# Optimization experiments

Measured on AMD Instinct MI355X. Metric: run time of the kernel, lower is better.

## Reference

```python
import jax, jax.numpy as jnp
import numpy as np

B, C, T, H, W = 32, 384, 16, 14, 14
K, NUM_SAMPLES, SIGMA = 8, 1000, 0.05
C2 = 2 * C  # ScoreNet doubles embed_dim internally


def setup_inputs() -> dict:
    key = jax.random.key(0)
    ks = jax.random.split(key, 12)
    def rn(k, shape, s=0.02):
        return jax.random.normal(k, shape, dtype=jnp.float32) * s
    return {
        "frames": jax.random.normal(ks[0], (B, C, T, H, W), dtype=jnp.float32),
        "noise": jax.random.normal(ks[1], (B, NUM_SAMPLES, T), dtype=jnp.float32),
        "conv_w": rn(ks[2], (C, C, 1, 3, 3)),
        "conv_b": jnp.zeros((C,), jnp.float32),
        "bn_g": jnp.ones((C,), jnp.float32),
        "bn_b": jnp.zeros((C,), jnp.float32),
        "ln_g": jnp.ones((C2,), jnp.float32),
        "ln_b": jnp.zeros((C2,), jnp.float32),
        "lin_w": rn(ks[3], (C2, C2)),
        "lin_b": jnp.zeros((C2,), jnp.float32),
        "w1": rn(ks[4], (C2, C)), "b1": jnp.zeros((C,), jnp.float32),
        "w2": rn(ks[5], (C, C // 2)), "b2": jnp.zeros((C // 2,), jnp.float32),
        "w3": rn(ks[6], (C // 2, 1)), "b3": jnp.zeros((1,), jnp.float32),
    }


def score_net(frames, conv_w, conv_b, bn_g, bn_b, ln_g, ln_b, lin_w, lin_b,
              w1, b1, w2, b2, w3, b3):
    x = jax.lax.stop_gradient(frames)  # ScoreNet detaches its input
    x = jax.lax.conv_general_dilated(
        x, conv_w, window_strides=(1, 2, 2), padding='VALID',
        dimension_numbers=('NCDHW', 'OIDHW', 'NCDHW'))
    x = x + conv_b[None, :, None, None, None]
    # BatchNorm3d in training mode: biased batch stats over (N,T,H,W)
    m = x.mean(axis=(0, 2, 3, 4))
    v = x.var(axis=(0, 2, 3, 4))
    x = (x - m[None, :, None, None, None]) / jnp.sqrt(v + 1e-5)[None, :, None, None, None]
    x = x * bn_g[None, :, None, None, None] + bn_b[None, :, None, None, None]
    # b c t h w -> b t (h w) c
    b, c, t, h, w = x.shape
    x = jnp.transpose(x, (0, 2, 3, 4, 1)).reshape(b, t, h * w, c)
    x = jnp.concatenate([x.mean(axis=2), x.max(axis=2)], axis=-1)  # [B,T,2C]
    # LayerNorm(2C)
    mu = x.mean(-1, keepdims=True)
    var = x.var(-1, keepdims=True)
    x = (x - mu) / jnp.sqrt(var + 1e-5) * ln_g + ln_b
    x = jax.nn.gelu(x @ lin_w + lin_b, approximate=False)
    local_x = x[..., :C2 // 2]
    global_x = jnp.broadcast_to(x[..., C2 // 2:].mean(axis=1, keepdims=True), (b, t, C2 // 2))
    x = jnp.concatenate([local_x, global_x], axis=-1)
    x = jax.nn.gelu(x @ w1 + b1, approximate=False)
    x = jax.nn.gelu(x @ w2 + b2, approximate=False)
    score = (x @ w3 + b3)[..., 0]  # [B,T]
    smin = score.min(axis=-1, keepdims=True)
    smax = score.max(axis=-1, keepdims=True)
    return (score - smin) / (smax - smin + 1e-5)


def perturbed_indicators(score, noise):
    d = score.shape[-1]
    pert = score[:, None, :] + noise * SIGMA  # [B,N,T]
    idx_top = jnp.sort(jax.lax.top_k(pert, K)[1], axis=-1)        # [B,N,K]
    idx_back = jnp.sort(jax.lax.top_k(-pert, d - K)[1], axis=-1)  # [B,N,T-K]
    ind_top = jax.nn.one_hot(idx_top, d, dtype=jnp.float32).mean(axis=1)   # [B,K,T]
    ind_back = jax.nn.one_hot(idx_back, d, dtype=jnp.float32).mean(axis=1)  # [B,T-K,T]
    return ind_top, ind_back


def reference(frames, noise, conv_w, conv_b, bn_g, bn_b, ln_g, ln_b, lin_w, lin_b,
              w1, b1, w2, b2, w3, b3):
    score = score_net(frames, conv_w, conv_b, bn_g, bn_b, ln_g, ln_b, lin_w, lin_b,
                      w1, b1, w2, b2, w3, b3)  # [B,T]
    ind_top, ind_back = perturbed_indicators(score, noise)
    # b c t h w -> b t (h w c)
    flat = jnp.transpose(frames, (0, 2, 3, 4, 1)).reshape(B, T, H * W * C)
    p_top = jnp.einsum('bkd,bdc->bkc', ind_top, flat)
    p_back = jnp.einsum('bkd,bdc->bkc', ind_back, flat)
    frames_topk = jnp.transpose(p_top.reshape(B, K, H, W, C), (0, 4, 1, 2, 3))
    frames_back = jnp.transpose(p_back.reshape(B, T - K, H, W, C), (0, 4, 1, 2, 3))
    sorted_inds = jnp.argsort(score, axis=1)
    return frames_topk, frames_back, sorted_inds
```

## Files before the change

### kernel.cpp

```cpp
#include <hip/hip_runtime.h>
#include <hip/hip_bf16.h>
#include <cstdint>

#define NB 32
#define NC 384
#define NT 16
#define NH 14
#define NW 14
#define HWI 196
#define HOW 6
#define HWO 36
#define C2 768
#define MCONV (NB*NT*HWO)
#define KCONV 3456
#define TOPK 8
#define NSAMP 1000
#define OUT_TOPK_ELEMS (NB*NC*TOPK*HWI)
#define OUT_INDS_OFF   (2*OUT_TOPK_ELEMS)
#define PELEMS (MCONV*NC)

#define OFF_FHI  0ull
#define OFF_FLO  77070336ull
#define OFF_WHI  154140672ull
#define OFF_WLO  156794880ull
#define OFF_CONV 159449088ull
#define OFF_PART 0ull
#define OFF_BNSC 442368ull
#define OFF_BNSH 443904ull
#define OFF_Y    445440ull
#define OFF_X1   2018304ull
#define OFF_GM   3591168ull
#define OFF_H1   3640320ull
#define OFF_H2   4426752ull
#define OFF_IND  4819968ull

typedef __attribute__((ext_vector_type(4))) float f32x4;
typedef __attribute__((ext_vector_type(8))) short bf16x8;

__device__ __forceinline__ unsigned short f2bf(float f) {
  unsigned u = __float_as_uint(f);
  unsigned r = (u + 0x7FFFu + ((u >> 16) & 1u)) >> 16;
  return (unsigned short)r;
}
__device__ __forceinline__ float bf2f(unsigned short u) {
  return __uint_as_float(((unsigned)u) << 16);
}

__device__ __forceinline__ void gload_lds16(const void* gptr, void* lptr) {
  __builtin_amdgcn_global_load_lds(
      (const __attribute__((address_space(1))) unsigned int*)gptr,
      (__attribute__((address_space(3))) unsigned int*)lptr, 16, 0, 0);
}

__global__ __launch_bounds__(256)
void split_all(const float* __restrict__ fr, const float* __restrict__ cw,
               unsigned short* __restrict__ fhi, unsigned short* __restrict__ flo,
               unsigned short* __restrict__ whi, unsigned short* __restrict__ wlo) {
  __shared__ char smem[64 * 197 * 4];
  int bid = blockIdx.x;
  if (bid < 3072) {
    unsigned int (*tile)[197] = (unsigned int (*)[197])smem;
    int cb = bid % 6, bt = bid / 6;
    int b = bt >> 4, t = bt & 15;
    const float* src = fr + (((size_t)b * NC + cb * 64) * NT + t) * HWI;
    for (int i = threadIdx.x; i < 64 * 49; i += 256) {
      int c = i / 49, q = i - c * 49;
      float4 v = *(const float4*)(src + (size_t)c * (NT * HWI) + q * 4);
      float vv[4] = {v.x, v.y, v.z, v.w};
#pragma unroll
      for (int u = 0; u < 4; ++u) {
        unsigned short h = f2bf(vv[u]);
        unsigned short l = f2bf(vv[u] - bf2f(h));
        tile[c][q * 4 + u] = ((unsigned)h << 16) | (unsigned)l;
      }
    }
    __syncthreads();
    size_t obase = ((size_t)bt * HWI) * NC + cb * 64;
    for (int i = threadIdx.x; i < 196 * 8; i += 256) {
      int hw = i >> 3, c8 = i & 7;
      bf16x8 vh, vl;
#pragma unroll
      for (int u = 0; u < 8; ++u) {
        unsigned p = tile[c8 * 8 + u][hw];
        vh[u] = (short)(p >> 16);
        vl[u] = (short)(p & 0xffff);
      }
      size_t o = obase + (size_t)hw * NC + c8 * 8;
      *(bf16x8*)(fhi + o) = vh;
      *(bf16x8*)(flo + o) = vl;
    }
  } else {
    float* t = (float*)smem;
    int co = bid - 3072;
    const float* src = cw + (size_t)co * KCONV;
    for (int i = threadIdx.x; i < KCONV / 4; i += 256)
      *(float4*)&t[i * 4] = *(const float4*)&src[i * 4];
    __syncthreads();
    unsigned short* oh = whi + (size_t)co * KCONV;
    unsigned short* ol = wlo + (size_t)co * KCONV;
    for (int i = threadIdx.x; i < KCONV; i += 256) {
      int c9 = i / NC, ci = i - c9 * NC;
      float v = t[ci * 9 + c9];
      unsigned short h = f2bf(v);
      oh[i] = h; ol[i] = f2bf(v - bf2f(h));
    }
  }
}

__global__ __launch_bounds__(256, 4)
void conv_gemm(const unsigned short* __restrict__ fhi,
               const unsigned short* __restrict__ flo,
               const unsigned short* __restrict__ whi,
               const unsigned short* __restrict__ wlo,
               const float* __restrict__ conv_b,
               float* __restrict__ p0, float* __restrict__ p1,
               float* __restrict__ p2, float* __restrict__ p3) {
  __shared__ unsigned short sAhi[128 * 32], sAlo[128 * 32];
  __shared__ unsigned short sBhi[128 * 32], sBlo[128 * 32];
  const int tid = threadIdx.x;
  const int lane = tid & 63;
  const int wv = tid >> 6;
  const int bid = blockIdx.x;
  const int bm = bid % 144;
  const int r  = bid / 144;
  const int bn = r % 3;
  const int kz = r / 3;

  int aoff[2], boff[2];
#pragma unroll
  for (int j = 0; j < 2; ++j) {
    int l = (wv * 2 + j) * 64 + lane;
    int row = l >> 2;
    int chunk = (l & 3) ^ ((l >> 3) & 3);
    int m = bm * 128 + row;
    int wo = m % 6; int tmp = m / 6;
    int ho = tmp % 6; tmp /= 6;
    aoff[j] = ((tmp * HWI) + (2 * ho) * NW + 2 * wo) * NC + chunk * 8;
    int co = bn * 128 + row;
    boff[j] = co * KCONV + chunk * 8;
  }

  f32x4 acc[4][4];
#pragma unroll
  for (int i = 0; i < 4; ++i)
#pragma unroll
    for (int j = 0; j < 4; ++j) acc[i][j] = (f32x4){0.f, 0.f, 0.f, 0.f};

  const int wrow = (wv >> 1) * 64;
  const int wcol = (wv & 1) * 64;
  const int fr_row = lane & 15;
  const int slot8 = (((lane >> 4) ^ ((fr_row >> 1) & 3))) * 8;

  int c9  = (kz * 27) / 12;
  int rem = (kz * 27) % 12;
  for (int s = 0; s < 27; ++s) {
    int kh = c9 / 3, kw = c9 - kh * 3;
    int soffA = (kh * NW + kw) * NC + rem * 32;
    int soffB = c9 * NC + rem * 32;
#pragma unroll
    for (int j = 0; j < 2; ++j) {
      char* ldsA  = (char*)sAhi + (wv * 2 + j) * 1024;
      char* ldsAl = (char*)sAlo + (wv * 2 + j) * 1024;
      char* ldsB  = (char*)sBhi + (wv * 2 + j) * 1024;
      char* ldsBl = (char*)sBlo + (wv * 2 + j) * 1024;
      gload_lds16(fhi + aoff[j] + soffA, ldsA);
      gload_lds16(flo + aoff[j] + soffA, ldsAl);
      gload_lds16(whi + boff[j] + soffB, ldsB);
      gload_lds16(wlo + boff[j] + soffB, ldsBl);
    }
    __syncthreads();
    bf16x8 ah[4], al[4], bh[4], bl[4];
#pragma unroll
    for (int m = 0; m < 4; ++m) {
      int rr = wrow + m * 16 + fr_row;
      ah[m] = *(const bf16x8*)&sAhi[rr * 32 + slot8];
      al[m] = *(const bf16x8*)&sAlo[rr * 32 + slot8];
    }
#pragma unroll
    for (int n = 0; n < 4; ++n) {
      int rr = wcol + n * 16 + fr_row;
      bh[n] = *(const bf16x8*)&sBhi[rr * 32 + slot8];
      bl[n] = *(const bf16x8*)&sBlo[rr * 32 + slot8];
    }
#pragma unroll
    for (int m = 0; m < 4; ++m)
#pragma unroll
      for (int n = 0; n < 4; ++n) {
        acc[m][n] = __builtin_amdgcn_mfma_f32_16x16x32_bf16(ah[m], bh[n], acc[m][n], 0, 0, 0);
        acc[m][n] = __builtin_amdgcn_mfma_f32_16x16x32_bf16(ah[m], bl[n], acc[m][n], 0, 0, 0);
        acc[m][n] = __builtin_amdgcn_mfma_f32_16x16x32_bf16(al[m], bh[n], acc[m][n], 0, 0, 0);
      }
    __syncthreads();
    if (++rem == 12) { rem = 0; ++c9; }
  }

  float* dst = (kz == 0) ? p0 : (kz == 1) ? p1 : (kz == 2) ? p2 : p3;
#pragma unroll
  for (int m = 0; m < 4; ++m)
#pragma unroll
    for (int n = 0; n < 4; ++n) {
      int col = bn * 128 + wcol + n * 16 + (lane & 15);
      float cb = (kz == 0) ? conv_b[col] : 0.f;
#pragma unroll
      for (int j = 0; j < 4; ++j) {
        int row = bm * 128 + wrow + m * 16 + (lane >> 4) * 4 + j;
        dst[(size_t)row * NC + col] = acc[m][n][j] + cb;
      }
    }
}

__global__ __launch_bounds__(384)
void bn_part(float* __restrict__ p0, const float* __restrict__ p1,
             const float* __restrict__ p2, const float* __restrict__ p3,
             float* __restrict__ part) {
  int c = threadIdx.x;
  int r0 = blockIdx.x * 128;
  float s = 0.f, sq = 0.f;
  for (int r = 0; r < 128; ++r) {
    size_t off = (size_t)(r0 + r) * NC + c;
    float v = p0[off] + p1[off] + p2[off] + p3[off];
    p0[off] = v;
    s += v; sq += v * v;
  }
  part[blockIdx.x * 768 + c] = s;
  part[blockIdx.x * 768 + 384 + c] = sq;
}

__global__ __launch_bounds__(384)
void bn_fin(const float* __restrict__ part, const float* __restrict__ bn_g,
            const float* __restrict__ bn_b, float* __restrict__ bnsc,
            float* __restrict__ bnsh) {
  int c = threadIdx.x;
  float s = 0.f, sq = 0.f;
  for (int i = 0; i < 144; ++i) {
    s += part[i * 768 + c];
    sq += part[i * 768 + 384 + c];
  }
  float mean = s / (float)MCONV;
  float var = sq / (float)MCONV - mean * mean;
  float sc = bn_g[c] / sqrtf(var + 1e-5f);
  bnsc[c] = sc;
  bnsh[c] = bn_b[c] - mean * sc;
}

__global__ __launch_bounds__(384)
void pool_ln(const float* __restrict__ csum,
             const float* __restrict__ bnsc,
             const float* __restrict__ bnsh, const float* __restrict__ ln_g,
             const float* __restrict__ ln_b, float* __restrict__ y) {
  __shared__ float r1[6], r2[6], stats[2];
  int bt = blockIdx.x, c = threadIdx.x;
  float sc = bnsc[c], sh = bnsh[c];
  size_t base = (size_t)bt * HWO * NC + c;
  float sum = 0.f, mx = -1e30f;
#pragma unroll
  for (int hw = 0; hw < HWO; ++hw) {
    float v = csum[base + (size_t)hw * NC] * sc + sh;
    sum += v;
    mx = fmaxf(mx, v);
  }
  float meanv = sum * (1.f / 36.f);
  float v1 = meanv + mx;
  float v2 = meanv * meanv + mx * mx;
#pragma unroll
  for (int off = 32; off; off >>= 1) {
    v1 += __shfl_down(v1, off, 64);
    v2 += __shfl_down(v2, off, 64);
  }
  if ((c & 63) == 0) { r1[c >> 6] = v1; r2[c >> 6] = v2; }
  __syncthreads();
  if (c == 0) {
    float S1 = 0.f, S2 = 0.f;
#pragma unroll
    for (int i = 0; i < 6; ++i) { S1 += r1[i]; S2 += r2[i]; }
    float mu = S1 / (float)C2;
    float var = S2 / (float)C2 - mu * mu;
    stats[0] = mu;
    stats[1] = 1.0f / sqrtf(var + 1e-5f);
  }
  __syncthreads();
  float mu = stats[0], rstd = stats[1];
  y[(size_t)bt * C2 + c] = (meanv - mu) * rstd * ln_g[c] + ln_b[c];
  y[(size_t)bt * C2 + 384 + c] = (mx - mu) * rstd * ln_g[384 + c] + ln_b[384 + c];
}

template <int GELU, int X2, int GM>
__global__ __launch_bounds__(256)
void gemm64(const float* __restrict__ A, const float* __restrict__ gmv,
            const float* __restrict__ Wm,
            const float* __restrict__ bias, float* __restrict__ Cm,
            int K, int N, float* __restrict__ gmout) {
  __shared__ float As[64][17];
  __shared__ float Bs[16][68];
  __shared__ float gmred[16][64];
  int tid = threadIdx.x;
  int tx = tid & 15, ty = tid >> 4;
  int m0 = blockIdx.y * 64, n0 = blockIdx.x * 64;
  int ar = tid >> 2, ak = (tid & 3) * 4;
  int br = tid >> 4, bc = (tid & 15) * 4;
  float acc[4][4] = {};
  for (int kt = 0; kt < K; kt += 16) {
    int kcol = kt + ak;
    float4 av;
    if (X2 && kcol >= 384)
      av = *(const float4*)(gmv + ((m0 + ar) >> 4) * 384 + (kcol - 384));
    else
      av = *(const float4*)(A + (size_t)(m0 + ar) * K + kcol);
    float4 bv = *(const float4*)(Wm + (size_t)(kt + br) * N + n0 + bc);
    As[ar][ak + 0] = av.x; As[ar][ak + 1] = av.y;
    As[ar][ak + 2] = av.z; As[ar][ak + 3] = av.w;
    Bs[br][bc + 0] = bv.x; Bs[br][bc + 1] = bv.y;
    Bs[br][bc + 2] = bv.z; Bs[br][bc + 3] = bv.w;
    __syncthreads();
#pragma unroll
    for (int kk = 0; kk < 16; ++kk) {
      float a0 = As[ty * 4 + 0][kk], a1 = As[ty * 4 + 1][kk];
      float a2 = As[ty * 4 + 2][kk], a3 = As[ty * 4 + 3][kk];
      float b0 = Bs[kk][tx * 4 + 0], b1 = Bs[kk][tx * 4 + 1];
      float b2 = Bs[kk][tx * 4 + 2], b3 = Bs[kk][tx * 4 + 3];
      acc[0][0] += a0 * b0; acc[0][1] += a0 * b1; acc[0][2] += a0 * b2; acc[0][3] += a0 * b3;
      acc[1][0] += a1 * b0; acc[1][1] += a1 * b1; acc[1][2] += a1 * b2; acc[1][3] += a1 * b3;
      acc[2][0] += a2 * b0; acc[2][1] += a2 * b1; acc[2][2] += a2 * b2; acc[2][3] += a2 * b3;
      acc[3][0] += a3 * b0; acc[3][1] += a3 * b1; acc[3][2] += a3 * b2; acc[3][3] += a3 * b3;
    }
    __syncthreads();
  }
  float vout[4][4];
#pragma unroll
  for (int i = 0; i < 4; ++i) {
    int row = m0 + ty * 4 + i;
#pragma unroll
    for (int j = 0; j < 4; ++j) {
      int col = n0 + tx * 4 + j;
      float v = acc[i][j] + bias[col];
      if (GELU) v = 0.5f * v * (1.0f + erff(v * 0.70710678118654752f));
      vout[i][j] = v;
      Cm[(size_t)row * N + col] = v;
    }
  }
  if (GM && n0 >= 384) {
#pragma unroll
    for (int j = 0; j < 4; ++j)
      gmred[ty][tx * 4 + j] = vout[0][j] + vout[1][j] + vout[2][j] + vout[3][j];
    __syncthreads();
    int b_l = tid >> 6, col = tid & 63;
    float g = (gmred[b_l * 4 + 0][col] + gmred[b_l * 4 + 1][col] +
               gmred[b_l * 4 + 2][col] + gmred[b_l * 4 + 3][col]) * (1.f / 16.f);
    gmout[(blockIdx.y * 4 + b_l) * 384 + (n0 - 384) + col] = g;
  }
}

__global__ __launch_bounds__(256)
void score_head(const float* __restrict__ h2, const float* __restrict__ w3,
                const float* __restrict__ b3, const float* __restrict__ noise,
                float* __restrict__ ind, float* __restrict__ out_inds) {
  int b = blockIdx.x;
  int tid = threadIdx.x;
  int lane = tid & 63, wv = tid >> 6;
  __shared__ float sv[16], sn[16];
  __shared__ unsigned cnt[256];
  for (int t = wv; t < 16; t += 4) {
    const float* hr = h2 + ((size_t)b * 16 + t) * 192;
    float p = 0.f;
    for (int i = lane; i < 192; i += 64) p += hr[i] * w3[i];
#pragma unroll
    for (int off = 32; off; off >>= 1) p += __shfl_down(p, off, 64);
    if (lane == 0) sv[t] = p + b3[0];
  }
  cnt[tid] = 0;
  __syncthreads();
  if (tid == 0) {
    float mn = sv[0], mx = sv[0];
    for (int t = 1; t < 16; ++t) { mn = fminf(mn, sv[t]); mx = fmaxf(mx, sv[t]); }
    float inv = 1.0f / (mx - mn + 1e-5f);
    for (int t = 0; t < 16; ++t) sn[t] = (sv[t] - mn) * inv;
  }
  __syncthreads();
  if (tid < 16) {
    int t = tid, r = 0;
    for (int u = 0; u < 16; ++u)
      r += (sv[u] < sv[t]) || (sv[u] == sv[t] && u < t);
    out_inds[b * 16 + r] = (float)t;
  }
  for (int s = tid; s < NSAMP; s += 256) {
    const float* nz = noise + ((size_t)b * NSAMP + s) * 16;
    float pert[16];
#pragma unroll
    for (int t = 0; t < 16; ++t) pert[t] = sn[t] + 0.05f * nz[t];
    unsigned tm = 0, bm2 = 0;
#pragma unroll
    for (int t = 0; t < 16; ++t) {
      int ct = 0, cb = 0;
#pragma unroll
      for (int u = 0; u < 16; ++u) {
        ct += (pert[u] > pert[t]) || (pert[u] == pert[t] && u < t);
        cb += (pert[u] < pert[t]) || (pert[u] == pert[t] && u < t);
      }
      if (ct < 8) tm |= 1u << t;
      if (cb < 8) bm2 |= 1u << t;
    }
    int j = 0, jb = 0;
#pragma unroll
    for (int t = 0; t < 16; ++t) {
      if (tm & (1u << t)) { if (j < 8) atomicAdd(&cnt[j * 16 + t], 1u); ++j; }
      if (bm2 & (1u << t)) { if (jb < 8) atomicAdd(&cnt[128 + jb * 16 + t], 1u); ++jb; }
    }
  }
  __syncthreads();
  ind[b * 256 + tid] = (float)cnt[tid] / 1000.0f;
}

__global__ __launch_bounds__(256)
void gather_k(const float* __restrict__ frames, const float* __restrict__ ind,
              float* __restrict__ out) {
  int bid = blockIdx.x;
  int tid = threadIdx.x;
  int b = (bid * 4) / NC;
  __shared__ float wt[256];
  wt[tid] = ind[b * 256 + tid];
  __syncthreads();
  if (tid >= 196) return;
  int cc = tid / 49, q = tid - cc * 49;
  int bc = bid * 4 + cc;
  const float4* src = (const float4*)(frames + (size_t)bc * NT * HWI) + q;
  float4 v[16];
#pragma unroll
  for (int t = 0; t < 16; ++t) v[t] = src[t * 49];
  float4* o1 = (float4*)(out + (size_t)bc * TOPK * HWI) + q;
  float4* o2 = (float4*)(out + OUT_TOPK_ELEMS + (size_t)bc * TOPK * HWI) + q;
#pragma unroll
  for (int k = 0; k < TOPK; ++k) {
    float4 st = {0.f, 0.f, 0.f, 0.f}, sb = {0.f, 0.f, 0.f, 0.f};
#pragma unroll
    for (int t = 0; t < 16; ++t) {
      float a = wt[k * 16 + t], bw = wt[128 + k * 16 + t];
      st.x += a * v[t].x; st.y += a * v[t].y; st.z += a * v[t].z; st.w += a * v[t].w;
      sb.x += bw * v[t].x; sb.y += bw * v[t].y; sb.z += bw * v[t].z; sb.w += bw * v[t].w;
    }
    o1[k * 49] = st;
    o2[k * 49] = sb;
  }
}

extern "C" void kernel_launch(void* const* d_in, const int* in_sizes, int n_in,
                              void* d_out, int out_size, void* d_ws, size_t ws_size,
                              hipStream_t stream) {
  const float* frames = (const float*)d_in[0];
  const float* noise  = (const float*)d_in[1];
  const float* conv_w = (const float*)d_in[2];
  const float* conv_b = (const float*)d_in[3];
  const float* bn_g   = (const float*)d_in[4];
  const float* bn_b   = (const float*)d_in[5];
  const float* ln_g   = (const float*)d_in[6];
  const float* ln_b   = (const float*)d_in[7];
  const float* lin_w  = (const float*)d_in[8];
  const float* lin_b  = (const float*)d_in[9];
  const float* w1     = (const float*)d_in[10];
  const float* b1     = (const float*)d_in[11];
  const float* w2     = (const float*)d_in[12];
  const float* b2     = (const float*)d_in[13];
  const float* w3     = (const float*)d_in[14];
  const float* b3     = (const float*)d_in[15];

  char* ws = (char*)d_ws;
  unsigned short* fhi = (unsigned short*)(ws + OFF_FHI);
  unsigned short* flo = (unsigned short*)(ws + OFF_FLO);
  unsigned short* whi = (unsigned short*)(ws + OFF_WHI);
  unsigned short* wlo = (unsigned short*)(ws + OFF_WLO);
  float* p0    = (float*)(ws + OFF_CONV);
  float* part  = (float*)(ws + OFF_PART);
  float* bnsc  = (float*)(ws + OFF_BNSC);
  float* bnsh  = (float*)(ws + OFF_BNSH);
  float* y     = (float*)(ws + OFF_Y);
  float* x1    = (float*)(ws + OFF_X1);
  float* gm    = (float*)(ws + OFF_GM);
  float* h1    = (float*)(ws + OFF_H1);
  float* h2    = (float*)(ws + OFF_H2);
  float* ind   = (float*)(ws + OFF_IND);
  float* out   = (float*)d_out;
  float* p1    = out;
  float* p2    = out + PELEMS;
  float* p3    = out + 2 * (size_t)PELEMS;

  split_all<<<3456, 256, 0, stream>>>(frames, conv_w, fhi, flo, whi, wlo);
  conv_gemm<<<1728, 256, 0, stream>>>(fhi, flo, whi, wlo, conv_b, p0, p1, p2, p3);
  bn_part<<<144, 384, 0, stream>>>(p0, p1, p2, p3, part);
  bn_fin<<<1, 384, 0, stream>>>(part, bn_g, bn_b, bnsc, bnsh);
  pool_ln<<<512, 384, 0, stream>>>(p0, bnsc, bnsh, ln_g, ln_b, y);
  gemm64<1, 0, 1><<<dim3(12, 8), 256, 0, stream>>>(y, nullptr, lin_w, lin_b, x1, 768, 768, gm);
  gemm64<1, 1, 0><<<dim3(6, 8), 256, 0, stream>>>(x1, gm, w1, b1, h1, 768, 384, nullptr);
  gemm64<1, 0, 0><<<dim3(3, 8), 256, 0, stream>>>(h1, nullptr, w2, b2, h2, 384, 192, nullptr);
  score_head<<<32, 256, 0, stream>>>(h2, w3, b3, noise, ind, out + OUT_INDS_OFF);
  gather_k<<<3072, 256, 0, stream>>>(frames, ind, out);
}
```

Before: 508.8 us.

## Fuse split-K reduction with pooling stats, remap conv blocks, split score sampling

The split-K partial sums are now reduced in a per-(b,t) kernel that also emits per-channel sum, sum of squares, max and min. This removes the write-back of the reduced conv output and the second full read in pool_ln, which now applies the BN affine to the pooled stats and picks max or min depending on the scale's sign. The conv GEMM block index is remapped so neighbouring blocks land differently across the hardware, and score_head is split across 8 blocks per batch with partial counts summed in gather_k. The sign trick relies on BN being monotone per channel, and bn_fin now reads 512 partial rows instead of 144.

```diff
diff --git a/kernel.cpp b/kernel.cpp
--- a/kernel.cpp
+++ b/kernel.cpp
@@ -24,15 +24,18 @@
 #define OFF_WHI  154140672ull
 #define OFF_WLO  156794880ull
 #define OFF_CONV 159449088ull
-#define OFF_PART 0ull
-#define OFF_BNSC 442368ull
-#define OFF_BNSH 443904ull
-#define OFF_Y    445440ull
-#define OFF_X1   2018304ull
-#define OFF_GM   3591168ull
-#define OFF_H1   3640320ull
-#define OFF_H2   4426752ull
-#define OFF_IND  4819968ull
+#define OFF_SARR 0ull
+#define OFF_SQAR 786432ull
+#define OFF_MXAR 1572864ull
+#define OFF_MNAR 2359296ull
+#define OFF_BNSC 3145728ull
+#define OFF_BNSH 3147264ull
+#define OFF_Y    3148800ull
+#define OFF_X1   4721664ull
+#define OFF_GM   6294528ull
+#define OFF_H1   6343680ull
+#define OFF_H2   7130112ull
+#define OFF_PCNT 7523328ull
 
 typedef __attribute__((ext_vector_type(4))) float f32x4;
 typedef __attribute__((ext_vector_type(8))) short bf16x8;
@@ -121,8 +124,10 @@
   const int lane = tid & 63;
   const int wv = tid >> 6;
   const int bid = blockIdx.x;
-  const int bm = bid % 144;
-  const int r  = bid / 144;
+  const int x  = bid & 7;
+  const int i_ = bid >> 3;
+  const int bm = x * 18 + (i_ % 18);
+  const int r  = i_ / 18;
   const int bn = r % 3;
   const int kz = r / 3;
 
@@ -210,31 +215,34 @@
 }
 
 __global__ __launch_bounds__(384)
-void bn_part(float* __restrict__ p0, const float* __restrict__ p1,
-             const float* __restrict__ p2, const float* __restrict__ p3,
-             float* __restrict__ part) {
-  int c = threadIdx.x;
-  int r0 = blockIdx.x * 128;
-  float s = 0.f, sq = 0.f;
-  for (int r = 0; r < 128; ++r) {
-    size_t off = (size_t)(r0 + r) * NC + c;
+void reduce_all(const float* __restrict__ p0, const float* __restrict__ p1,
+                const float* __restrict__ p2, const float* __restrict__ p3,
+                float* __restrict__ sarr, float* __restrict__ sqarr,
+                float* __restrict__ mxarr, float* __restrict__ mnarr) {
+  int bt = blockIdx.x, c = threadIdx.x;
+  size_t base = (size_t)bt * HWO * NC + c;
+  float s = 0.f, sq = 0.f, mx = -3.4e38f, mn = 3.4e38f;
+#pragma unroll 6
+  for (int hw = 0; hw < HWO; ++hw) {
+    size_t off = base + (size_t)hw * NC;
     float v = p0[off] + p1[off] + p2[off] + p3[off];
-    p0[off] = v;
     s += v; sq += v * v;
-  }
-  part[blockIdx.x * 768 + c] = s;
-  part[blockIdx.x * 768 + 384 + c] = sq;
+    mx = fmaxf(mx, v); mn = fminf(mn, v);
+  }
+  int o = bt * NC + c;
+  sarr[o] = s; sqarr[o] = sq; mxarr[o] = mx; mnarr[o] = mn;
 }
 
 __global__ __launch_bounds__(384)
-void bn_fin(const float* __restrict__ part, const float* __restrict__ bn_g,
-            const float* __restrict__ bn_b, float* __restrict__ bnsc,
-            float* __restrict__ bnsh) {
+void bn_fin(const float* __restrict__ sarr, const float* __restrict__ sqarr,
+            const float* __restrict__ bn_g, const float* __restrict__ bn_b,
+            float* __restrict__ bnsc, float* __restrict__ bnsh) {
   int c = threadIdx.x;
   float s = 0.f, sq = 0.f;
-  for (int i = 0; i < 144; ++i) {
-    s += part[i * 768 + c];
-    sq += part[i * 768 + 384 + c];
+#pragma unroll 8
+  for (int i = 0; i < 512; ++i) {
+    s += sarr[i * NC + c];
+    sq += sqarr[i * NC + c];
   }
   float mean = s / (float)MCONV;
   float var = sq / (float)MCONV - mean * mean;
@@ -244,24 +252,19 @@
 }
 
 __global__ __launch_bounds__(384)
-void pool_ln(const float* __restrict__ csum,
-             const float* __restrict__ bnsc,
-             const float* __restrict__ bnsh, const float* __restrict__ ln_g,
-             const float* __restrict__ ln_b, float* __restrict__ y) {
+void pool_ln(const float* __restrict__ sarr, const float* __restrict__ mxarr,
+             const float* __restrict__ mnarr,
+             const float* __restrict__ bnsc, const float* __restrict__ bnsh,
+             const float* __restrict__ ln_g, const float* __restrict__ ln_b,
+             float* __restrict__ y) {
   __shared__ float r1[6], r2[6], stats[2];
   int bt = blockIdx.x, c = threadIdx.x;
+  int o = bt * NC + c;
   float sc = bnsc[c], sh = bnsh[c];
-  size_t base = (size_t)bt * HWO * NC + c;
-  float sum = 0.f, mx = -1e30f;
-#pragma unroll
-  for (int hw = 0; hw < HWO; ++hw) {
-    float v = csum[base + (size_t)hw * NC] * sc + sh;
-    sum += v;
-    mx = fmaxf(mx, v);
-  }
-  float meanv = sum * (1.f / 36.f);
-  float v1 = meanv + mx;
-  float v2 = meanv * meanv + mx * mx;
+  float meanv = sarr[o] * (1.f / 36.f) * sc + sh;
+  float mxv = (sc >= 0.f ? mxarr[o] : mnarr[o]) * sc + sh;
+  float v1 = meanv + mxv;
+  float v2 = meanv * meanv + mxv * mxv;
 #pragma unroll
   for (int off = 32; off; off >>= 1) {
     v1 += __shfl_down(v1, off, 64);
@@ -281,7 +284,7 @@
   __syncthreads();
   float mu = stats[0], rstd = stats[1];
   y[(size_t)bt * C2 + c] = (meanv - mu) * rstd * ln_g[c] + ln_b[c];
-  y[(size_t)bt * C2 + 384 + c] = (mx - mu) * rstd * ln_g[384 + c] + ln_b[384 + c];
+  y[(size_t)bt * C2 + 384 + c] = (mxv - mu) * rstd * ln_g[384 + c] + ln_b[384 + c];
 }
 
 template <int GELU, int X2, int GM>
@@ -353,8 +356,8 @@
 __global__ __launch_bounds__(256)
 void score_head(const float* __restrict__ h2, const float* __restrict__ w3,
                 const float* __restrict__ b3, const float* __restrict__ noise,
-                float* __restrict__ ind, float* __restrict__ out_inds) {
-  int b = blockIdx.x;
+                unsigned* __restrict__ pcnt, float* __restrict__ out_inds) {
+  int b = blockIdx.x >> 3, chunk = blockIdx.x & 7;
   int tid = threadIdx.x;
   int lane = tid & 63, wv = tid >> 6;
   __shared__ float sv[16], sn[16];
@@ -376,13 +379,14 @@
     for (int t = 0; t < 16; ++t) sn[t] = (sv[t] - mn) * inv;
   }
   __syncthreads();
-  if (tid < 16) {
+  if (chunk == 0 && tid < 16) {
     int t = tid, r = 0;
     for (int u = 0; u < 16; ++u)
       r += (sv[u] < sv[t]) || (sv[u] == sv[t] && u < t);
     out_inds[b * 16 + r] = (float)t;
   }
-  for (int s = tid; s < NSAMP; s += 256) {
+  if (tid < 125) {
+    int s = chunk * 125 + tid;
     const float* nz = noise + ((size_t)b * NSAMP + s) * 16;
     float pert[16];
 #pragma unroll
@@ -407,17 +411,23 @@
     }
   }
   __syncthreads();
-  ind[b * 256 + tid] = (float)cnt[tid] / 1000.0f;
+  pcnt[(size_t)(b * 8 + chunk) * 256 + tid] = cnt[tid];
 }
 
 __global__ __launch_bounds__(256)
-void gather_k(const float* __restrict__ frames, const float* __restrict__ ind,
+void gather_k(const float* __restrict__ frames, const unsigned* __restrict__ pcnt,
               float* __restrict__ out) {
   int bid = blockIdx.x;
   int tid = threadIdx.x;
   int b = (bid * 4) / NC;
   __shared__ float wt[256];
-  wt[tid] = ind[b * 256 + tid];
+  {
+    unsigned s = 0;
+    const unsigned* pc = pcnt + (size_t)b * 8 * 256 + tid;
+#pragma unroll
+    for (int ch = 0; ch < 8; ++ch) s += pc[ch * 256];
+    wt[tid] = (float)s / 1000.0f;
+  }
   __syncthreads();
   if (tid >= 196) return;
   int cc = tid / 49, q = tid - cc * 49;
@@ -468,7 +478,10 @@
   unsigned short* whi = (unsigned short*)(ws + OFF_WHI);
   unsigned short* wlo = (unsigned short*)(ws + OFF_WLO);
   float* p0    = (float*)(ws + OFF_CONV);
-  float* part  = (float*)(ws + OFF_PART);
+  float* sarr  = (float*)(ws + OFF_SARR);
+  float* sqarr = (float*)(ws + OFF_SQAR);
+  float* mxarr = (float*)(ws + OFF_MXAR);
+  float* mnarr = (float*)(ws + OFF_MNAR);
   float* bnsc  = (float*)(ws + OFF_BNSC);
   float* bnsh  = (float*)(ws + OFF_BNSH);
   float* y     = (float*)(ws + OFF_Y);
@@ -476,7 +489,7 @@
   float* gm    = (float*)(ws + OFF_GM);
   float* h1    = (float*)(ws + OFF_H1);
   float* h2    = (float*)(ws + OFF_H2);
-  float* ind   = (float*)(ws + OFF_IND);
+  unsigned* pcnt = (unsigned*)(ws + OFF_PCNT);
   float* out   = (float*)d_out;
   float* p1    = out;
   float* p2    = out + PELEMS;
@@ -484,12 +497,12 @@
 
   split_all<<<3456, 256, 0, stream>>>(frames, conv_w, fhi, flo, whi, wlo);
   conv_gemm<<<1728, 256, 0, stream>>>(fhi, flo, whi, wlo, conv_b, p0, p1, p2, p3);
-  bn_part<<<144, 384, 0, stream>>>(p0, p1, p2, p3, part);
-  bn_fin<<<1, 384, 0, stream>>>(part, bn_g, bn_b, bnsc, bnsh);
-  pool_ln<<<512, 384, 0, stream>>>(p0, bnsc, bnsh, ln_g, ln_b, y);
+  reduce_all<<<512, 384, 0, stream>>>(p0, p1, p2, p3, sarr, sqarr, mxarr, mnarr);
+  bn_fin<<<1, 384, 0, stream>>>(sarr, sqarr, bn_g, bn_b, bnsc, bnsh);
+  pool_ln<<<512, 384, 0, stream>>>(sarr, mxarr, mnarr, bnsc, bnsh, ln_g, ln_b, y);
   gemm64<1, 0, 1><<<dim3(12, 8), 256, 0, stream>>>(y, nullptr, lin_w, lin_b, x1, 768, 768, gm);
   gemm64<1, 1, 0><<<dim3(6, 8), 256, 0, stream>>>(x1, gm, w1, b1, h1, 768, 384, nullptr);
   gemm64<1, 0, 0><<<dim3(3, 8), 256, 0, stream>>>(h1, nullptr, w2, b2, h2, 384, 192, nullptr);
-  score_head<<<32, 256, 0, stream>>>(h2, w3, b3, noise, ind, out + OUT_INDS_OFF);
-  gather_k<<<3072, 256, 0, stream>>>(frames, ind, out);
-}
+  score_head<<<256, 256, 0, stream>>>(h2, w3, b3, noise, pcnt, out + OUT_INDS_OFF);
+  gather_k<<<3072, 256, 0, stream>>>(frames, pcnt, out);
+}
```

New measurement: 512.0 us. No clear change (+0.6%).
